# Kernel tuning notes

Hardware: AMD Instinct MI355X
Metric: run time of the kernel (lower is better)

The kernel has to match this reference:

```python
import jax, jax.numpy as jnp
import numpy as np

N_EMBD = 1024
N_HEAD = 16
HEAD_DIM = N_EMBD // N_HEAD


def setup_inputs() -> dict:
    key = jax.random.key(0)
    k1, k2, k3, k4, k5 = jax.random.split(key, 5)
    B, T, C = 4, 2048, N_EMBD
    s = 1.0 / np.sqrt(C)
    return {
        "x": jax.random.normal(k1, (B, T, C), dtype=jnp.float32),
        "W_attn": jax.random.normal(k2, (C, 3 * C), dtype=jnp.float32) * s,
        "b_attn": jnp.zeros((3 * C,), dtype=jnp.float32),
        "W_proj": jax.random.normal(k3, (C, C), dtype=jnp.float32) * s,
        "b_proj": jnp.zeros((C,), dtype=jnp.float32),
    }


def reference(x, W_attn, b_attn, W_proj, b_proj):
    B, T, C = x.shape
    H, D = N_HEAD, HEAD_DIM
    # fused QKV projection
    qkv = x @ W_attn + b_attn                       # [B,T,3C]
    q, k, v = jnp.split(qkv, 3, axis=2)
    q = q.reshape(B, T, H, D).transpose(0, 2, 1, 3)  # [B,H,T,D]
    k = k.reshape(B, T, H, D).transpose(0, 2, 1, 3)
    v = v.reshape(B, T, H, D).transpose(0, 2, 1, 3)
    # causal scaled dot-product attention
    scale = 1.0 / jnp.sqrt(jnp.asarray(D, dtype=x.dtype))
    scores = jnp.einsum('bhqd,bhkd->bhqk', q, k) * scale  # [B,H,T,T]
    causal = jnp.tril(jnp.ones((T, T), dtype=bool))
    scores = jnp.where(causal[None, None], scores, jnp.finfo(x.dtype).min)
    attn = jax.nn.softmax(scores, axis=-1)
    y = jnp.einsum('bhqk,bhkd->bhqd', attn, v)      # [B,H,T,D]
    y = y.transpose(0, 2, 1, 3).reshape(B, T, C)
    return y @ W_proj + b_proj
```

## Files before the change

### kernel.cpp

```cpp
#include <hip/hip_runtime.h>
#include <hip/hip_bf16.h>
#include <cstdint>

#define B_ 4
#define T_ 2048
#define C_ 1024
#define H_ 16
#define D_ 64
#define M_ (B_*T_)
#define N3 (3*C_)

typedef __bf16 bf16;
typedef __bf16 bf16x8 __attribute__((ext_vector_type(8)));
typedef __bf16 bf16x4 __attribute__((ext_vector_type(4)));
typedef float  floatx4 __attribute__((ext_vector_type(4)));

__device__ __forceinline__ void gl_lds16(const bf16* g, bf16* l) {
  __builtin_amdgcn_global_load_lds(
      (__attribute__((address_space(1))) void*)(void*)g,
      (__attribute__((address_space(3))) void*)(void*)l,
      16, 0, 0);
}

__global__ void cast_to_bf16(const float* __restrict__ in, bf16* __restrict__ out, int n) {
  int i = (blockIdx.x * blockDim.x + threadIdx.x) * 4;
  if (i < n) {
    const float4 f = *(const float4*)(in + i);
    bf16x4 o;
    o.x = (bf16)f.x; o.y = (bf16)f.y; o.z = (bf16)f.z; o.w = (bf16)f.w;
    *(bf16x4*)(out + i) = o;
  }
}

__global__ void transpose_cast(const float* __restrict__ in, bf16* __restrict__ out,
                               int R, int C) {
  __shared__ float tile[32][33];
  int r0 = blockIdx.y * 32, c0 = blockIdx.x * 32;
  int tx = threadIdx.x & 31, ty = threadIdx.x >> 5;
  #pragma unroll
  for (int j = 0; j < 32; j += 8)
    tile[ty + j][tx] = in[(size_t)(r0 + ty + j) * C + c0 + tx];
  __syncthreads();
  #pragma unroll
  for (int j = 0; j < 32; j += 8)
    out[(size_t)(c0 + ty + j) * R + r0 + tx] = (bf16)tile[tx][ty + j];
}

__global__ __launch_bounds__(256)
void transpose_v(const bf16* __restrict__ in, bf16* __restrict__ out) {
  __shared__ __attribute__((aligned(16))) bf16 tileN[64 * 64];
  const int tid = threadIdx.x;
  const int bh = blockIdx.z;
  const int t0 = blockIdx.x * 64;
  const int sk = tid >> 2, scc = tid & 3;
  {
    const bf16* p = in + ((size_t)bh * T_ + t0 + sk) * D_ + scc * 16;
    const bf16x8 r0 = *(const bf16x8*)p;
    const bf16x8 r1 = *(const bf16x8*)(p + 8);
    *(bf16x8*)(tileN + sk * 64 + ((2 * scc)     ^ (sk & 7)) * 8) = r0;
    *(bf16x8*)(tileN + sk * 64 + ((2 * scc + 1) ^ (sk & 7)) * 8) = r1;
  }
  __syncthreads();
  const int tc = (tid & 7) * 8;
  #pragma unroll
  for (int half = 0; half < 2; half++) {
    const int d = (tid >> 3) + half * 32;
    bf16x8 o;
    #pragma unroll
    for (int j = 0; j < 8; j++)
      o[j] = tileN[(tc + j) * 64 + (((d >> 3) ^ j) * 8) + (d & 7)];
    *(bf16x8*)(out + ((size_t)bh * D_ + d) * T_ + t0 + tc) = o;
  }
}

template<int MODE>
__global__ __launch_bounds__(256)
void gemm_bt(const bf16* __restrict__ A, const bf16* __restrict__ Bt,
             const float* __restrict__ bias, float* __restrict__ out,
             bf16* __restrict__ qo, bf16* __restrict__ ko, bf16* __restrict__ vo,
             int M, int N, int K)
{
  __shared__ __attribute__((aligned(16))) bf16 As[128 * 32];
  __shared__ __attribute__((aligned(16))) bf16 Bs[128 * 32];

  const int tid  = threadIdx.x;
  const int w    = tid >> 6;
  const int lane = tid & 63;
  const int quad = lane >> 4;
  const int l16  = lane & 15;
  const int wm   = w & 1, wn = w >> 1;
  const int m0   = blockIdx.y * 128, n0 = blockIdx.x * 128;

  floatx4 acc[4][4] = {};

  const int lrow = lane >> 2;
  const int lk   = (lane & 3) * 8;

  const bf16* aptr = A  + (size_t)(m0 + w * 32 + lrow) * K + lk;
  const bf16* bptr = Bt + (size_t)(n0 + w * 32 + lrow) * K + lk;
  bf16* asl = As + w * 1024;
  bf16* bsl = Bs + w * 1024;

  for (int k0 = 0; k0 < K; k0 += 32) {
    gl_lds16(aptr,          asl);
    gl_lds16(aptr + 16 * K, asl + 512);
    gl_lds16(bptr,          bsl);
    gl_lds16(bptr + 16 * K, bsl + 512);
    aptr += 32; bptr += 32;
    __syncthreads();

    bf16x8 af[4], bfb[4];
    #pragma unroll
    for (int i = 0; i < 4; i++)
      af[i] = *(const bf16x8*)(As + (wm * 64 + i * 16 + l16) * 32 + quad * 8);
    #pragma unroll
    for (int i = 0; i < 4; i++)
      bfb[i] = *(const bf16x8*)(Bs + (wn * 64 + i * 16 + l16) * 32 + quad * 8);
    #pragma unroll
    for (int mi = 0; mi < 4; mi++)
      #pragma unroll
      for (int ni = 0; ni < 4; ni++)
        acc[mi][ni] = __builtin_amdgcn_mfma_f32_16x16x32_bf16(af[mi], bfb[ni], acc[mi][ni], 0, 0, 0);
    __syncthreads();
  }

  #pragma unroll
  for (int mi = 0; mi < 4; mi++) {
    #pragma unroll
    for (int ni = 0; ni < 4; ni++) {
      const int col = n0 + wn * 64 + ni * 16 + l16;
      const float bv = bias[col];
      #pragma unroll
      for (int r = 0; r < 4; r++) {
        const int row = m0 + wm * 64 + mi * 16 + quad * 4 + r;
        const float val = acc[mi][ni][r] + bv;
        if (MODE == 0) {
          const int b = row >> 11, t = row & 2047;
          const int s = col >> 10, c = col & 1023;
          const int h = c >> 6,  d = c & 63;
          bf16* dst = (s == 0) ? qo : (s == 1) ? ko : vo;
          dst[((size_t)(b * H_ + h) * T_ + t) * D_ + d] = (bf16)val;
        } else {
          out[(size_t)row * N + col] = val;
        }
      }
    }
  }
}

__global__ __launch_bounds__(256)
void attn_kernel(const bf16* __restrict__ Q, const bf16* __restrict__ Kp,
                 const bf16* __restrict__ Vt, bf16* __restrict__ Y)
{
  __shared__ __attribute__((aligned(16))) bf16 Ks[64 * 72];
  __shared__ __attribute__((aligned(16))) bf16 Vs[64 * 72];
  __shared__ __attribute__((aligned(16))) bf16 Ps[4][16 * 72];

  const int tid  = threadIdx.x;
  const int w    = tid >> 6, lane = tid & 63;
  const int quad = lane >> 4, l16 = lane & 15;
  const int bh = blockIdx.y;
  const int b = bh >> 4, h = bh & 15;

  const int sk = tid >> 2;
  const int sc = (tid & 3) * 16;

  const bf16* Kbase = Kp + (size_t)bh * T_ * D_;
  const bf16* Vbase = Vt + (size_t)bh * D_ * T_;

  const float SC = 0.125f * 1.44269504088896f;

  #pragma unroll 1
  for (int tix = 0; tix < 2; tix++) {
    const int qt = (tix == 0) ? (15 - blockIdx.x) : blockIdx.x;
    const int q0 = qt * 128;
    const int nch = 2 * qt + 2;

    bf16x8 qf[2][2];
    #pragma unroll
    for (int mt = 0; mt < 2; mt++) {
      const bf16* qp = Q + ((size_t)bh * T_ + q0 + mt * 64 + w * 16 + l16) * D_ + quad * 8;
      qf[mt][0] = *(const bf16x8*)qp;
      qf[mt][1] = *(const bf16x8*)(qp + 32);
    }

    floatx4 o[2][4] = {};
    float l_r[2][4] = {};

    bf16x8 ka0, ka1, va0, va1, kb0, kb1, vb0, vb1;
    {
      const bf16* kp = Kbase + (size_t)sk * D_ + sc;
      ka0 = *(const bf16x8*)kp; ka1 = *(const bf16x8*)(kp + 8);
      const bf16* vp = Vbase + (size_t)sk * T_ + sc;
      va0 = *(const bf16x8*)vp; va1 = *(const bf16x8*)(vp + 8);
    }

    #pragma unroll 1
    for (int c = 0; c < nch; c++) {
      __syncthreads();
      if ((c & 1) == 0) {
        *(bf16x8*)(Ks + sk * 72 + sc)     = ka0;
        *(bf16x8*)(Ks + sk * 72 + sc + 8) = ka1;
        *(bf16x8*)(Vs + sk * 72 + sc)     = va0;
        *(bf16x8*)(Vs + sk * 72 + sc + 8) = va1;
        if (c + 1 < nch) {
          const bf16* kp = Kbase + (size_t)((c + 1) * 64 + sk) * D_ + sc;
          kb0 = *(const bf16x8*)kp; kb1 = *(const bf16x8*)(kp + 8);
          const bf16* vp = Vbase + (size_t)sk * T_ + (c + 1) * 64 + sc;
          vb0 = *(const bf16x8*)vp; vb1 = *(const bf16x8*)(vp + 8);
        }
      } else {
        *(bf16x8*)(Ks + sk * 72 + sc)     = kb0;
        *(bf16x8*)(Ks + sk * 72 + sc + 8) = kb1;
        *(bf16x8*)(Vs + sk * 72 + sc)     = vb0;
        *(bf16x8*)(Vs + sk * 72 + sc + 8) = vb1;
        if (c + 1 < nch) {
          const bf16* kp = Kbase + (size_t)((c + 1) * 64 + sk) * D_ + sc;
          ka0 = *(const bf16x8*)kp; ka1 = *(const bf16x8*)(kp + 8);
          const bf16* vp = Vbase + (size_t)sk * T_ + (c + 1) * 64 + sc;
          va0 = *(const bf16x8*)vp; va1 = *(const bf16x8*)(vp + 8);
        }
      }
      __syncthreads();

      const int kv0 = c * 64;
      const bool act0 = (c < nch - 1);

      floatx4 s[2][4];
      #pragma unroll
      for (int nt = 0; nt < 4; nt++) {
        const bf16x8 kf0 = *(const bf16x8*)(Ks + (nt * 16 + l16) * 72 + quad * 8);
        const bf16x8 kf1 = *(const bf16x8*)(Ks + (nt * 16 + l16) * 72 + 32 + quad * 8);
        if (act0) {
          floatx4 z = {};
          z = __builtin_amdgcn_mfma_f32_16x16x32_bf16(qf[0][0], kf0, z, 0, 0, 0);
          s[0][nt] = __builtin_amdgcn_mfma_f32_16x16x32_bf16(qf[0][1], kf1, z, 0, 0, 0);
        }
        floatx4 z = {};
        z = __builtin_amdgcn_mfma_f32_16x16x32_bf16(qf[1][0], kf0, z, 0, 0, 0);
        s[1][nt] = __builtin_amdgcn_mfma_f32_16x16x32_bf16(qf[1][1], kf1, z, 0, 0, 0);
      }

      bf16x8 vfr[4][2];
      #pragma unroll
      for (int nt = 0; nt < 4; nt++) {
        const uint32_t* vrow = (const uint32_t*)Vs + (size_t)(nt * 16 + l16) * 36;
        #pragma unroll
        for (int hf = 0; hf < 2; hf++) {
          const uint32_t w0 = vrow[hf * 4 + quad];
          const uint32_t w1 = vrow[hf * 4 + quad + 8];
          const uint32_t w2 = vrow[hf * 4 + quad + 16];
          const uint32_t w3 = vrow[hf * 4 + quad + 24];
          union { uint32_t u[4]; bf16x8 v; } U;
          U.u[0] = (w0 & 0xffffu) | (w1 << 16);
          U.u[1] = (w2 & 0xffffu) | (w3 << 16);
          U.u[2] = (w0 >> 16) | (w1 & 0xffff0000u);
          U.u[3] = (w2 >> 16) | (w3 & 0xffff0000u);
          vfr[nt][hf] = U.v;
        }
      }

      #pragma unroll
      for (int mt = 0; mt < 2; mt++) {
        if (mt == 0 && !act0) continue;
        const bool diag = (c == 2 * qt + mt);
        #pragma unroll
        for (int r = 0; r < 4; r++) {
          const int qrow = q0 + mt * 64 + w * 16 + quad * 4 + r;
          float x0 = s[mt][0][r], x1 = s[mt][1][r], x2 = s[mt][2][r], x3 = s[mt][3][r];
          if (diag) {
            if (kv0      + l16 > qrow) x0 = -1e30f;
            if (kv0 + 16 + l16 > qrow) x1 = -1e30f;
            if (kv0 + 32 + l16 > qrow) x2 = -1e30f;
            if (kv0 + 48 + l16 > qrow) x3 = -1e30f;
          }
          const float e0 = exp2f(fmaf(x0, SC, -8.f));
          const float e1 = exp2f(fmaf(x1, SC, -8.f));
          const float e2 = exp2f(fmaf(x2, SC, -8.f));
          const float e3 = exp2f(fmaf(x3, SC, -8.f));
          l_r[mt][r] += (e0 + e1) + (e2 + e3);
          bf16x4 pv;
          pv.x = (bf16)e0; pv.y = (bf16)e1; pv.z = (bf16)e2; pv.w = (bf16)e3;
          *(bf16x4*)(&Ps[w][(quad * 4 + r) * 72 + l16 * 4]) = pv;
        }
        const bf16x8 pf0 = *(const bf16x8*)(&Ps[w][l16 * 72 + quad * 8]);
        const bf16x8 pf1 = *(const bf16x8*)(&Ps[w][l16 * 72 + 32 + quad * 8]);
        #pragma unroll
        for (int nt = 0; nt < 4; nt++) {
          o[mt][nt] = __builtin_amdgcn_mfma_f32_16x16x32_bf16(pf0, vfr[nt][0], o[mt][nt], 0, 0, 0);
          o[mt][nt] = __builtin_amdgcn_mfma_f32_16x16x32_bf16(pf1, vfr[nt][1], o[mt][nt], 0, 0, 0);
        }
      }
    }

    #pragma unroll
    for (int mt = 0; mt < 2; mt++) {
      #pragma unroll
      for (int r = 0; r < 4; r++) {
        float ls = l_r[mt][r];
        ls += __shfl_xor(ls, 1);
        ls += __shfl_xor(ls, 2);
        ls += __shfl_xor(ls, 4);
        ls += __shfl_xor(ls, 8);
        const float inv = 1.f / ls;
        const int t = q0 + mt * 64 + w * 16 + quad * 4 + r;
        #pragma unroll
        for (int nt = 0; nt < 4; nt++)
          Y[((size_t)b * T_ + t) * C_ + h * D_ + nt * 16 + l16] = (bf16)(o[mt][nt][r] * inv);
      }
    }
  }
}

extern "C" void kernel_launch(void* const* d_in, const int* in_sizes, int n_in,
                              void* d_out, int out_size, void* d_ws, size_t ws_size,
                              hipStream_t stream)
{
  const float* x      = (const float*)d_in[0];
  const float* W_attn = (const float*)d_in[1];
  const float* b_attn = (const float*)d_in[2];
  const float* W_proj = (const float*)d_in[3];
  const float* b_proj = (const float*)d_in[4];
  float* out = (float*)d_out;

  bf16* xb  = (bf16*)d_ws;
  bf16* wat = xb  + (size_t)M_ * C_;
  bf16* wpt = wat + (size_t)N3 * C_;
  bf16* qb  = wpt + (size_t)C_ * C_;
  bf16* kb  = qb  + (size_t)M_ * C_;
  bf16* vb  = kb  + (size_t)M_ * C_;
  bf16* yb  = vb  + (size_t)M_ * C_;
  bf16* vtb = xb;

  cast_to_bf16<<<dim3(M_ * C_ / 1024), 256, 0, stream>>>(x, xb, M_ * C_);
  transpose_cast<<<dim3(N3 / 32, C_ / 32), 256, 0, stream>>>(W_attn, wat, C_, N3);
  transpose_cast<<<dim3(C_ / 32, C_ / 32), 256, 0, stream>>>(W_proj, wpt, C_, C_);
  gemm_bt<0><<<dim3(N3 / 128, M_ / 128), 256, 0, stream>>>(
      xb, wat, b_attn, nullptr, qb, kb, vb, M_, N3, C_);
  transpose_v<<<dim3(T_ / 64, 1, B_ * H_), 256, 0, stream>>>(vb, vtb);
  attn_kernel<<<dim3(T_ / 256, B_ * H_), 256, 0, stream>>>(qb, kb, vtb, yb);
  gemm_bt<1><<<dim3(C_ / 128, M_ / 128), 256, 0, stream>>>(
      yb, wpt, b_proj, out, nullptr, nullptr, nullptr, M_, C_, C_);
}
```

Before: 296.4 us.

## Double-buffer K/V LDS tiles and pre-permute V transpose to drop register shuffles

```diff
diff --git a/kernel.cpp b/kernel.cpp
--- a/kernel.cpp
+++ b/kernel.cpp
@@ -67,8 +67,11 @@
     const int d = (tid >> 3) + half * 32;
     bf16x8 o;
     #pragma unroll
-    for (int j = 0; j < 8; j++)
-      o[j] = tileN[(tc + j) * 64 + (((d >> 3) ^ j) * 8) + (d & 7)];
+    for (int j = 0; j < 8; j++) {
+      const int slot = tc + j;
+      const int row = 16 * (slot & 3) + (slot >> 2);
+      o[j] = tileN[row * 64 + (((d >> 3) ^ (row & 7)) * 8) + (d & 7)];
+    }
     *(bf16x8*)(out + ((size_t)bh * D_ + d) * T_ + t0 + tc) = o;
   }
 }
@@ -150,10 +153,10 @@
 
 __global__ __launch_bounds__(256)
 void attn_kernel(const bf16* __restrict__ Q, const bf16* __restrict__ Kp,
-                 const bf16* __restrict__ Vt, bf16* __restrict__ Y)
+                 const bf16* __restrict__ Vtp, bf16* __restrict__ Y)
 {
-  __shared__ __attribute__((aligned(16))) bf16 Ks[64 * 72];
-  __shared__ __attribute__((aligned(16))) bf16 Vs[64 * 72];
+  __shared__ __attribute__((aligned(16))) bf16 Ks[2][64 * 72];
+  __shared__ __attribute__((aligned(16))) bf16 Vs[2][64 * 72];
   __shared__ __attribute__((aligned(16))) bf16 Ps[4][16 * 72];
 
   const int tid  = threadIdx.x;
@@ -165,14 +168,14 @@
   const int sk = tid >> 2;
   const int sc = (tid & 3) * 16;
 
-  const bf16* Kbase = Kp + (size_t)bh * T_ * D_;
-  const bf16* Vbase = Vt + (size_t)bh * D_ * T_;
+  const bf16* Kbase = Kp  + (size_t)bh * T_ * D_;
+  const bf16* Vbase = Vtp + (size_t)bh * D_ * T_;
 
   const float SC = 0.125f * 1.44269504088896f;
 
   #pragma unroll 1
   for (int tix = 0; tix < 2; tix++) {
-    const int qt = (tix == 0) ? (15 - blockIdx.x) : blockIdx.x;
+    const int qt = (tix == 0) ? (15 - (int)blockIdx.x) : (int)blockIdx.x;
     const int q0 = qt * 128;
     const int nch = 2 * qt + 2;
 
@@ -187,50 +190,41 @@
     floatx4 o[2][4] = {};
     float l_r[2][4] = {};
 
-    bf16x8 ka0, ka1, va0, va1, kb0, kb1, vb0, vb1;
     {
       const bf16* kp = Kbase + (size_t)sk * D_ + sc;
-      ka0 = *(const bf16x8*)kp; ka1 = *(const bf16x8*)(kp + 8);
+      const bf16x8 k0 = *(const bf16x8*)kp, k1 = *(const bf16x8*)(kp + 8);
       const bf16* vp = Vbase + (size_t)sk * T_ + sc;
-      va0 = *(const bf16x8*)vp; va1 = *(const bf16x8*)(vp + 8);
-    }
+      const bf16x8 v0 = *(const bf16x8*)vp, v1 = *(const bf16x8*)(vp + 8);
+      bf16* kd = Ks[0] + sk * 72 + sc;
+      *(bf16x8*)kd = k0; *(bf16x8*)(kd + 8) = k1;
+      bf16* vd = Vs[0] + sk * 72 + sc;
+      *(bf16x8*)vd = v0; *(bf16x8*)(vd + 8) = v1;
+    }
+    __syncthreads();
 
     #pragma unroll 1
     for (int c = 0; c < nch; c++) {
-      __syncthreads();
-      if ((c & 1) == 0) {
-        *(bf16x8*)(Ks + sk * 72 + sc)     = ka0;
-        *(bf16x8*)(Ks + sk * 72 + sc + 8) = ka1;
-        *(bf16x8*)(Vs + sk * 72 + sc)     = va0;
-        *(bf16x8*)(Vs + sk * 72 + sc + 8) = va1;
-        if (c + 1 < nch) {
-          const bf16* kp = Kbase + (size_t)((c + 1) * 64 + sk) * D_ + sc;
-          kb0 = *(const bf16x8*)kp; kb1 = *(const bf16x8*)(kp + 8);
-          const bf16* vp = Vbase + (size_t)sk * T_ + (c + 1) * 64 + sc;
-          vb0 = *(const bf16x8*)vp; vb1 = *(const bf16x8*)(vp + 8);
-        }
-      } else {
-        *(bf16x8*)(Ks + sk * 72 + sc)     = kb0;
-        *(bf16x8*)(Ks + sk * 72 + sc + 8) = kb1;
-        *(bf16x8*)(Vs + sk * 72 + sc)     = vb0;
-        *(bf16x8*)(Vs + sk * 72 + sc + 8) = vb1;
-        if (c + 1 < nch) {
-          const bf16* kp = Kbase + (size_t)((c + 1) * 64 + sk) * D_ + sc;
-          ka0 = *(const bf16x8*)kp; ka1 = *(const bf16x8*)(kp + 8);
-          const bf16* vp = Vbase + (size_t)sk * T_ + (c + 1) * 64 + sc;
-          va0 = *(const bf16x8*)vp; va1 = *(const bf16x8*)(vp + 8);
-        }
-      }
-      __syncthreads();
-
+      const int cur = c & 1;
+
+      bf16x8 nk0, nk1, nv0, nv1;
+      const bool have = (c + 1 < nch);
+      if (have) {
+        const bf16* kp = Kbase + (size_t)((c + 1) * 64 + sk) * D_ + sc;
+        nk0 = *(const bf16x8*)kp; nk1 = *(const bf16x8*)(kp + 8);
+        const bf16* vp = Vbase + (size_t)sk * T_ + (c + 1) * 64 + sc;
+        nv0 = *(const bf16x8*)vp; nv1 = *(const bf16x8*)(vp + 8);
+      }
+
+      const bf16* KsC = Ks[cur];
+      const bf16* VsC = Vs[cur];
       const int kv0 = c * 64;
       const bool act0 = (c < nch - 1);
 
       floatx4 s[2][4];
       #pragma unroll
       for (int nt = 0; nt < 4; nt++) {
-        const bf16x8 kf0 = *(const bf16x8*)(Ks + (nt * 16 + l16) * 72 + quad * 8);
-        const bf16x8 kf1 = *(const bf16x8*)(Ks + (nt * 16 + l16) * 72 + 32 + quad * 8);
+        const bf16x8 kf0 = *(const bf16x8*)(KsC + (nt * 16 + l16) * 72 + quad * 8);
+        const bf16x8 kf1 = *(const bf16x8*)(KsC + (nt * 16 + l16) * 72 + 32 + quad * 8);
         if (act0) {
           floatx4 z = {};
           z = __builtin_amdgcn_mfma_f32_16x16x32_bf16(qf[0][0], kf0, z, 0, 0, 0);
@@ -244,20 +238,8 @@
       bf16x8 vfr[4][2];
       #pragma unroll
       for (int nt = 0; nt < 4; nt++) {
-        const uint32_t* vrow = (const uint32_t*)Vs + (size_t)(nt * 16 + l16) * 36;
-        #pragma unroll
-        for (int hf = 0; hf < 2; hf++) {
-          const uint32_t w0 = vrow[hf * 4 + quad];
-          const uint32_t w1 = vrow[hf * 4 + quad + 8];
-          const uint32_t w2 = vrow[hf * 4 + quad + 16];
-          const uint32_t w3 = vrow[hf * 4 + quad + 24];
-          union { uint32_t u[4]; bf16x8 v; } U;
-          U.u[0] = (w0 & 0xffffu) | (w1 << 16);
-          U.u[1] = (w2 & 0xffffu) | (w3 << 16);
-          U.u[2] = (w0 >> 16) | (w1 & 0xffff0000u);
-          U.u[3] = (w2 >> 16) | (w3 & 0xffff0000u);
-          vfr[nt][hf] = U.v;
-        }
+        vfr[nt][0] = *(const bf16x8*)(VsC + (nt * 16 + l16) * 72 + quad * 8);
+        vfr[nt][1] = *(const bf16x8*)(VsC + (nt * 16 + l16) * 72 + 32 + quad * 8);
       }
 
       #pragma unroll
@@ -291,6 +273,14 @@
           o[mt][nt] = __builtin_amdgcn_mfma_f32_16x16x32_bf16(pf1, vfr[nt][1], o[mt][nt], 0, 0, 0);
         }
       }
+
+      if (have) {
+        bf16* kd = Ks[cur ^ 1] + sk * 72 + sc;
+        *(bf16x8*)kd = nk0; *(bf16x8*)(kd + 8) = nk1;
+        bf16* vd = Vs[cur ^ 1] + sk * 72 + sc;
+        *(bf16x8*)vd = nv0; *(bf16x8*)(vd + 8) = nv1;
+      }
+      __syncthreads();
     }
 
     #pragma unroll
```

After: 293.2 us. Within noise of the previous version (-1.1%).
